# Kernel tuning notes

Measured on AMD Instinct MI355X. Metric: run time of the kernel, lower is better.

## Reference

```python
import jax, jax.numpy as jnp
import numpy as np
from jax import lax

SIGMA1, SIGMA2, TRUNCATE = 4.2, 96.0, 4.0


def _gauss_kernel1d(sigma, truncate):
    # scipy-style: radius = int(truncate*sigma + 0.5), normalized Gaussian
    r = int(truncate * sigma + 0.5)
    t = jnp.arange(-r, r + 1, dtype=jnp.float32)
    k = jnp.exp(-0.5 * (t / sigma) ** 2)
    return k / jnp.sum(k)


def _depthwise_conv1d_centered(x_bcl, k):
    # x_bcl: [B, C, L]; k: [K] with K odd. Centered 'same' conv with reflect padding.
    B, C, L = x_bcl.shape
    K = k.shape[0]
    r = (K - 1) // 2
    xp = jnp.pad(x_bcl, ((0, 0), (0, 0), (r, r)), mode='reflect')
    w = jnp.broadcast_to(k[None, None, :], (C, 1, K)).astype(x_bcl.dtype)
    return lax.conv_general_dilated(
        xp, w, window_strides=(1,), padding='VALID',
        feature_group_count=C,
        dimension_numbers=('NCH', 'OIH', 'NCH'))


def setup_inputs() -> dict:
    key = jax.random.key(0)
    x = jax.random.normal(key, (32, 4096, 321), dtype=jnp.float32)  # [B, L, C]
    return {"x": x}


def reference(x) -> jnp.ndarray:
    k1 = _gauss_kernel1d(SIGMA1, TRUNCATE).astype(x.dtype)
    k2 = _gauss_kernel1d(SIGMA2, TRUNCATE).astype(x.dtype)
    x_bcl = jnp.transpose(x, (0, 2, 1))          # [B, C, L]
    y1 = _depthwise_conv1d_centered(x_bcl, k1)   # narrow Gaussian LP
    y2 = _depthwise_conv1d_centered(x_bcl, k2)   # wide Gaussian LP
    seasonal = y1 - y2
    return jnp.transpose(seasonal, (0, 2, 1))    # back to [B, L, C]
```

## Files before the change

### kernel.cpp

```cpp
#include <hip/hip_runtime.h>
#include <math.h>


#define Bdim 32
#define Ldim 4096
#define Cdim 321

#define R1 17
#define K1n 35
#define R2 384
#define K2n 769

#define GA_R 48
#define GA_N 97
#define GB_R 24
#define GB_N 49

#define NG 257
#define NJD 305
#define NGRP_A 20
#define NSEG 128
#define NTJ 33

#define GA_OFF 0
#define GB_OFF 128
#define W1_OFF 192
#define K2_OFF 256
#define K2P_OFF 1088
#define E2_OFF 4096
#define D_OFF 4096
#define E_OFF (D_OFF + Bdim*NJD*Cdim)
#define WS_TOT (E_OFF + Bdim*NG*Cdim)

__device__ __forceinline__ int mirror_idx(int a) {
    a = a < 0 ? -a : a;
    a = a > (Ldim - 1) ? 2 * (Ldim - 1) - a : a;
    return a;
}

__device__ __forceinline__ int xcd_swizzle(int bid, int nwg) {
    int q = nwg >> 3, r = nwg & 7;
    int xcd = bid & 7, i = bid >> 3;
    int base = (xcd < r) ? xcd * (q + 1) : r * (q + 1) + (xcd - r) * q;
    return base + i;
}

__device__ __forceinline__ float block_sum_1024(float v, float* partial) {
#pragma unroll
    for (int off = 32; off >= 1; off >>= 1) v += __shfl_down(v, off, 64);
    __syncthreads();
    if ((threadIdx.x & 63) == 0) partial[threadIdx.x >> 6] = v;
    __syncthreads();
    float s = partial[0];
#pragma unroll
    for (int i = 1; i < 16; ++i) s += partial[i];
    return s;
}

__global__ void init_weights_kernel(float* __restrict__ w) {
    __shared__ float partial[16];
    const int tid = threadIdx.x;

    {
        float v = 0.f;
        if (tid < GA_N) { float t = (float)(tid - GA_R) * (1.0f / 12.0f); v = expf(-0.5f * t * t); }
        float s = block_sum_1024(v, partial);
        if (tid < GA_N) w[GA_OFF + tid] = v / s;
    }
    {
        const float sb = sqrtf(96.f * 96.f - 12.f * 12.f) * (1.0f / 16.0f);
        float v = 0.f;
        if (tid < GB_N) { float t = (float)(tid - GB_R) / sb; v = expf(-0.5f * t * t); }
        float s = block_sum_1024(v, partial);
        if (tid < GB_N) w[GB_OFF + tid] = v / s;
    }
    {
        float v = 0.f;
        if (tid < K1n) { float t = (float)(tid - R1) * (1.0f / 4.2f); v = expf(-0.5f * t * t); }
        float s = block_sum_1024(v, partial);
        if (tid < K1n) w[W1_OFF + tid] = v / s;
    }
    {
        float v = 0.f;
        if (tid < K2n) { float t = (float)(tid - R2) * (1.0f / 96.0f); v = expf(-0.5f * t * t); }
        float s = block_sum_1024(v, partial);
        if (tid < K2n) w[K2_OFF + tid] = v / s;
        if (tid < 784) w[K2P_OFF + tid] = (tid < K2n) ? v / s : 0.f;
    }
}

__global__ __launch_bounds__(256) void decimA_kernel(
        const float* __restrict__ x, const float* __restrict__ ga,
        float* __restrict__ d) {
    __shared__ float gs[GA_N];
    if (threadIdx.x < GA_N) gs[threadIdx.x] = ga[threadIdx.x];
    __syncthreads();

    const int lb = xcd_swizzle(blockIdx.x, gridDim.x);
    const int lin = lb * 256 + threadIdx.x;
    const int c = lin % Cdim;
    const int rest = lin / Cdim;
    const int g = rest % NGRP_A;
    const int b = rest / NGRP_A;
    if (b >= Bdim) return;

    const int jj0 = -24 + 16 * g;
    const float* xb = x + b * (Ldim * Cdim) + c;

    float acc[16];
#pragma unroll
    for (int ii = 0; ii < 16; ++ii) acc[ii] = 0.f;

    const bool interior = (jj0 >= 3) && (jj0 <= 237);

#pragma unroll 1
    for (int p = 0; p < 16; ++p) {
        float row[22];
        if (interior) {
            const float* xp = xb + (16 * (jj0 - 3) + p) * Cdim;
#pragma unroll
            for (int i = 0; i < 22; ++i) row[i] = xp[i * (16 * Cdim)];
        } else {
#pragma unroll
            for (int i = 0; i < 22; ++i)
                row[i] = xb[mirror_idx(16 * (jj0 - 3 + i) + p) * Cdim];
        }
#pragma unroll
        for (int q = 0; q < 6; ++q) {
            const float wq = gs[16 * q + p];
#pragma unroll
            for (int ii = 0; ii < 16; ++ii)
                acc[ii] = fmaf(wq, row[ii + q], acc[ii]);
        }
        if (p == 0) {
            const float w6 = gs[96];
#pragma unroll
            for (int ii = 0; ii < 16; ++ii)
                acc[ii] = fmaf(w6, row[ii + 6], acc[ii]);
        }
    }

    const int j0d = jj0 + 24;
    float* db = d + (b * NJD + j0d) * Cdim + c;
#pragma unroll
    for (int ii = 0; ii < 16; ++ii)
        if (j0d + ii < NJD) db[ii * Cdim] = acc[ii];
}

__global__ __launch_bounds__(256) void coarseB_kernel(
        const float* __restrict__ d, const float* __restrict__ gb,
        float* __restrict__ e) {
    __shared__ float gbs[GB_N];
    if (threadIdx.x < GB_N) gbs[threadIdx.x] = gb[threadIdx.x];
    __syncthreads();

    const int lin = blockIdx.x * 256 + threadIdx.x;
    const int c = lin % Cdim;
    const int rest = lin / Cdim;
    const int tj = rest % NTJ;
    const int b = rest / NTJ;
    if (b >= Bdim) return;

    const int j0 = tj * 8;
    const float* db = d + b * (NJD * Cdim) + c;

    float row[56];
#pragma unroll
    for (int r = 0; r < 56; ++r) {
        int idx = j0 + r;
        idx = idx > (NJD - 1) ? (NJD - 1) : idx;
        row[r] = db[idx * Cdim];
    }

    float acc[8];
#pragma unroll
    for (int jj = 0; jj < 8; ++jj) acc[jj] = 0.f;
#pragma unroll
    for (int s = 0; s < GB_N; ++s) {
        const float wv = gbs[s];
#pragma unroll
        for (int jj = 0; jj < 8; ++jj)
            acc[jj] = fmaf(wv, row[s + jj], acc[jj]);
    }

    float* eb = e + (b * NG + j0) * Cdim + c;
#pragma unroll
    for (int jj = 0; jj < 8; ++jj)
        if (j0 + jj < NG) eb[jj * Cdim] = acc[jj];
}

__global__ __launch_bounds__(256, 2) void narrow_kernel(
        const float* __restrict__ x, const float* __restrict__ w1,
        const float* __restrict__ e, float* __restrict__ out) {
    __shared__ float ws[K1n];
    if (threadIdx.x < K1n) ws[threadIdx.x] = w1[threadIdx.x];
    __syncthreads();

    const int lb = xcd_swizzle(blockIdx.x, gridDim.x);
    const int lin = lb * 256 + threadIdx.x;
    const int c = lin % Cdim;
    const int rest = lin / Cdim;
    const int seg = rest % NSEG;
    const int b = rest / NSEG;
    if (b >= Bdim) return;

    const int l0 = seg * 32;
    const float* xb = x + b * (Ldim * Cdim) + c;

    const int j0 = seg * 2;
    const float* eb = e + (b * NG + j0) * Cdim + c;
    const float z0 = eb[0];
    const float z1 = eb[Cdim];
    const float z2 = eb[2 * Cdim];

    float row[66];
    if (seg >= 1 && seg <= 126) {
        const float* xp = xb + (l0 - R1) * Cdim;
#pragma unroll
        for (int i = 0; i < 66; ++i) row[i] = xp[i * Cdim];
    } else {
#pragma unroll
        for (int i = 0; i < 66; ++i)
            row[i] = xb[mirror_idx(l0 - R1 + i) * Cdim];
    }

    float acc[32];
#pragma unroll
    for (int m = 0; m < 32; ++m) acc[m] = 0.f;
#pragma unroll
    for (int t = 0; t < K1n; ++t) {
        const float wt = ws[t];
#pragma unroll
        for (int m = 0; m < 32; ++m)
            acc[m] = fmaf(wt, row[t + m], acc[m]);
    }

    const float d0 = (z1 - z0) * (1.0f / 16.0f);
    const float d1 = (z2 - z1) * (1.0f / 16.0f);
    float* ob = out + (b * Ldim + l0) * Cdim + c;
#pragma unroll
    for (int m = 0; m < 16; ++m)
        ob[m * Cdim] = acc[m] - fmaf(d0, (float)m, z0);
#pragma unroll
    for (int m = 16; m < 32; ++m)
        ob[m * Cdim] = acc[m] - fmaf(d1, (float)(m - 16), z1);
}

#define JPT 16
#define NJG 17
__global__ __launch_bounds__(256, 2) void wide_mid_kernel(
        const float* __restrict__ x, const float* __restrict__ w2p,
        float* __restrict__ z) {
    __shared__ float w2s[784];
    for (int i = threadIdx.x; i < 784; i += 256) w2s[i] = w2p[i];
    __syncthreads();

    const int gid = blockIdx.x * 256 + threadIdx.x;
    const int c = gid % Cdim;
    const int rest = gid / Cdim;
    const int jg = rest % NJG;
    const int b = rest / NJG;
    if (b >= Bdim) return;

    const int j0 = jg * JPT;
    const float* xb = x + b * (Ldim * Cdim) + c;

    float acc[JPT];
#pragma unroll
    for (int jj = 0; jj < JPT; ++jj) acc[jj] = 0.f;

    const bool interior = (j0 >= 24) && (16 * (j0 + 39) + 15 <= Ldim - 1);

#pragma unroll 1
    for (int p = 0; p < 16; ++p) {
        float row[64];
        if (interior) {
            const float* xp = xb + (16 * (j0 - 24) + p) * Cdim;
#pragma unroll
            for (int i = 0; i < 64; ++i) row[i] = xp[i * (16 * Cdim)];
        } else {
#pragma unroll
            for (int i = 0; i < 64; ++i)
                row[i] = xb[mirror_idx(16 * (j0 - 24 + i) + p) * Cdim];
        }
#pragma unroll
        for (int q = 0; q < 49; ++q) {
            const float wq = w2s[q * 16 + p];
#pragma unroll
            for (int jj = 0; jj < JPT; ++jj)
                acc[jj] = fmaf(wq, row[q + jj], acc[jj]);
        }
    }

    float* zb = z + (b * NG + j0) * Cdim + c;
#pragma unroll
    for (int jj = 0; jj < JPT; ++jj)
        if (j0 + jj < NG) zb[jj * Cdim] = acc[jj];
}

__global__ __launch_bounds__(256) void naive_kernel(
        const float* __restrict__ x, const float* __restrict__ w,
        float* __restrict__ out) {
    const int gid = blockIdx.x * 256 + threadIdx.x;
    if (gid >= Bdim * Ldim * Cdim) return;
    const int c = gid % Cdim;
    const int rest = gid / Cdim;
    const int l = rest % Ldim;
    const int b = rest / Ldim;
    const float* xb = x + b * (Ldim * Cdim) + c;
    float a2 = 0.f, a1 = 0.f;
    for (int t = 0; t < K2n; ++t)
        a2 = fmaf(w[K2_OFF + t], xb[mirror_idx(l + t - R2) * Cdim], a2);
#pragma unroll
    for (int t = 0; t < K1n; ++t)
        a1 = fmaf(w[W1_OFF + t], xb[mirror_idx(l + t - R1) * Cdim], a1);
    out[gid] = a1 - a2;
}

extern "C" void kernel_launch(void* const* d_in, const int* in_sizes, int n_in,
                              void* d_out, int out_size, void* d_ws, size_t ws_size,
                              hipStream_t stream) {
    (void)in_sizes; (void)n_in; (void)out_size;
    const float* x = (const float*)d_in[0];
    float* out = (float*)d_out;
    float* w = (float*)d_ws;

    hipLaunchKernelGGL(init_weights_kernel, dim3(1), dim3(1024), 0, stream, w);

    const size_t need_pyr = (size_t)WS_TOT * sizeof(float);
    const size_t need_mid = (size_t)(E2_OFF + Bdim * NG * Cdim) * sizeof(float);

    const int nar_total = Bdim * NSEG * Cdim;
    const dim3 nar_grid((nar_total + 255) / 256);

    if (ws_size >= need_pyr) {
        const int a_total = Bdim * NGRP_A * Cdim;
        hipLaunchKernelGGL(decimA_kernel, dim3((a_total + 255) / 256), dim3(256),
                           0, stream, x, w + GA_OFF, w + D_OFF);
        const int b_total = Bdim * NTJ * Cdim;
        hipLaunchKernelGGL(coarseB_kernel, dim3((b_total + 255) / 256), dim3(256),
                           0, stream, w + D_OFF, w + GB_OFF, w + E_OFF);
        hipLaunchKernelGGL(narrow_kernel, nar_grid, dim3(256),
                           0, stream, x, w + W1_OFF, w + E_OFF, out);
    } else if (ws_size >= need_mid) {
        const int wide_total = Bdim * NJG * Cdim;
        hipLaunchKernelGGL(wide_mid_kernel, dim3((wide_total + 255) / 256), dim3(256),
                           0, stream, x, w + K2P_OFF, w + E2_OFF);
        hipLaunchKernelGGL(narrow_kernel, nar_grid, dim3(256),
                           0, stream, x, w + W1_OFF, w + E2_OFF, out);
    } else {
        const int total = Bdim * Ldim * Cdim;
        hipLaunchKernelGGL(naive_kernel, dim3((total + 255) / 256), dim3(256),
                           0, stream, x, w, out);
    }
}
```

Before: 150.4 us.

## Stage narrow-filter input tiles in LDS via direct global-to-LDS loads

Replaces the narrow-filter kernel on the pyramid path with a tiled version. Each block stages a 66-row by 128-channel window of x into shared memory, using global_load_lds for the aligned channel tiles and a plain loop for the 65-channel tail. Each thread then computes 8 outputs for two channels with packed float2 FMAs from a register window. The wide-band value is linearly interpolated from the coarse pyramid level. This removes the redundant per-output global reads of the 35-tap window, at the cost of LDS use and higher register pressure.

```diff
diff --git a/kernel.cpp b/kernel.cpp
--- a/kernel.cpp
+++ b/kernel.cpp
@@ -19,8 +19,14 @@
 #define NG 257
 #define NJD 305
 #define NGRP_A 20
+#define NTJ 33
+
+#define TLN 32
+#define WR 66
+#define LSTR 128
+#define NLG3 128
+#define NCT3 3
 #define NSEG 128
-#define NTJ 33
 
 #define GA_OFF 0
 #define GB_OFF 128
@@ -32,6 +38,8 @@
 #define E_OFF (D_OFF + Bdim*NJD*Cdim)
 #define WS_TOT (E_OFF + Bdim*NG*Cdim)
 
+typedef float f32x2 __attribute__((ext_vector_type(2)));
+
 __device__ __forceinline__ int mirror_idx(int a) {
     a = a < 0 ? -a : a;
     a = a > (Ldim - 1) ? 2 * (Ldim - 1) - a : a;
@@ -189,7 +197,114 @@
         if (j0 + jj < NG) eb[jj * Cdim] = acc[jj];
 }
 
-__global__ __launch_bounds__(256, 2) void narrow_kernel(
+__global__ __launch_bounds__(256) void narrow_v10_kernel(
+        const float* __restrict__ x, const float* __restrict__ w1,
+        const float* __restrict__ e, float* __restrict__ out) {
+    __shared__ float ws[K1n];
+    __shared__ float tile[WR * LSTR];
+    if (threadIdx.x < K1n) ws[threadIdx.x] = w1[threadIdx.x];
+
+    const int bid = xcd_swizzle(blockIdx.x, gridDim.x);
+    const int ct = bid % NCT3;
+    const int rest = bid / NCT3;
+    const int lg = rest % NLG3;
+    const int b = rest / NLG3;
+
+    const int c0 = ct * 128;
+    const int l0 = lg * TLN;
+    const int lbase = l0 - R1;
+    const int lane = threadIdx.x & 63;
+    const int wv = threadIdx.x >> 6;
+    const float* xb = x + (size_t)b * (Ldim * Cdim);
+
+    if (ct < 2) {
+        const int rsel = (lane >> 5);
+        const int coff = (lane & 31) * 4;
+#pragma unroll
+        for (int k = 0; k < 9; ++k) {
+            const int p = wv + 4 * k;
+            if (p < 33) {
+                const int grow = mirror_idx(lbase + 2 * p + rsel);
+                const float* g = xb + (size_t)grow * Cdim + c0 + coff;
+                __builtin_amdgcn_global_load_lds(
+                    (const __attribute__((address_space(1))) void*)g,
+                    (__attribute__((address_space(3))) void*)(&tile[2 * p * LSTR]),
+                    16, 0, 0);
+            }
+        }
+    } else {
+#pragma unroll 1
+        for (int i = threadIdx.x; i < WR * 65; i += 256) {
+            const int r = i / 65;
+            const int cc = i - r * 65;
+            tile[r * LSTR + cc] = xb[(size_t)mirror_idx(lbase + r) * Cdim + 256 + cc];
+        }
+    }
+    __syncthreads();
+
+    const int cp = threadIdx.x & 63;
+    const int lgrp = threadIdx.x >> 6;
+    const int lg8 = lgrp * 8;
+    const int j = (l0 >> 4) + (lgrp >> 1);
+    const float f0 = (float)((lgrp & 1) * 8);
+
+    if (ct < 2 || cp < 32) {
+        f32x2 r2[42];
+#pragma unroll
+        for (int i = 0; i < 42; ++i)
+            r2[i] = *reinterpret_cast<const f32x2*>(&tile[(lg8 + i) * LSTR + 2 * cp]);
+
+        f32x2 acc[8];
+#pragma unroll
+        for (int m = 0; m < 8; ++m) acc[m] = (f32x2)(0.f);
+#pragma unroll
+        for (int t = 0; t < K1n; ++t) {
+            const float wt = ws[t];
+            const f32x2 w2 = {wt, wt};
+#pragma unroll
+            for (int m = 0; m < 8; ++m)
+                acc[m] = __builtin_elementwise_fma(w2, r2[t + m], acc[m]);
+        }
+
+        const int ce = c0 + 2 * cp;
+        const float* eb = e + ((size_t)b * NG + j) * Cdim + ce;
+        const float z0x = eb[0],    z0y = eb[1];
+        const float z1x = eb[Cdim], z1y = eb[Cdim + 1];
+        const float dzx = (z1x - z0x) * 0.0625f;
+        const float dzy = (z1y - z0y) * 0.0625f;
+
+        float* ob = out + ((size_t)b * Ldim + l0 + lg8) * Cdim + ce;
+#pragma unroll
+        for (int m = 0; m < 8; ++m) {
+            const float fm = f0 + (float)m;
+            ob[m * Cdim]     = acc[m].x - fmaf(dzx, fm, z0x);
+            ob[m * Cdim + 1] = acc[m].y - fmaf(dzy, fm, z0y);
+        }
+    } else if (cp == 32) {
+        float rs[42];
+#pragma unroll
+        for (int i = 0; i < 42; ++i) rs[i] = tile[(lg8 + i) * LSTR + 64];
+        float acc[8];
+#pragma unroll
+        for (int m = 0; m < 8; ++m) acc[m] = 0.f;
+#pragma unroll
+        for (int t = 0; t < K1n; ++t) {
+            const float wt = ws[t];
+#pragma unroll
+            for (int m = 0; m < 8; ++m)
+                acc[m] = fmaf(wt, rs[t + m], acc[m]);
+        }
+        const float z0 = e[((size_t)b * NG + j) * Cdim + 320];
+        const float z1 = e[((size_t)b * NG + j + 1) * Cdim + 320];
+        const float dz = (z1 - z0) * 0.0625f;
+        float* ob = out + ((size_t)b * Ldim + l0 + lg8) * Cdim + 320;
+#pragma unroll
+        for (int m = 0; m < 8; ++m)
+            ob[m * Cdim] = acc[m] - fmaf(dz, f0 + (float)m, z0);
+    }
+}
+
+__global__ __launch_bounds__(256, 2) void narrow_reg_kernel(
         const float* __restrict__ x, const float* __restrict__ w1,
         const float* __restrict__ e, float* __restrict__ out) {
     __shared__ float ws[K1n];
@@ -330,9 +445,6 @@
     const size_t need_pyr = (size_t)WS_TOT * sizeof(float);
     const size_t need_mid = (size_t)(E2_OFF + Bdim * NG * Cdim) * sizeof(float);
 
-    const int nar_total = Bdim * NSEG * Cdim;
-    const dim3 nar_grid((nar_total + 255) / 256);
-
     if (ws_size >= need_pyr) {
         const int a_total = Bdim * NGRP_A * Cdim;
         hipLaunchKernelGGL(decimA_kernel, dim3((a_total + 255) / 256), dim3(256),
@@ -340,13 +452,15 @@
         const int b_total = Bdim * NTJ * Cdim;
         hipLaunchKernelGGL(coarseB_kernel, dim3((b_total + 255) / 256), dim3(256),
                            0, stream, w + D_OFF, w + GB_OFF, w + E_OFF);
-        hipLaunchKernelGGL(narrow_kernel, nar_grid, dim3(256),
+        const int nblk = Bdim * NLG3 * NCT3;
+        hipLaunchKernelGGL(narrow_v10_kernel, dim3(nblk), dim3(256),
                            0, stream, x, w + W1_OFF, w + E_OFF, out);
     } else if (ws_size >= need_mid) {
         const int wide_total = Bdim * NJG * Cdim;
         hipLaunchKernelGGL(wide_mid_kernel, dim3((wide_total + 255) / 256), dim3(256),
                            0, stream, x, w + K2P_OFF, w + E2_OFF);
-        hipLaunchKernelGGL(narrow_kernel, nar_grid, dim3(256),
+        const int nar_total = Bdim * NSEG * Cdim;
+        hipLaunchKernelGGL(narrow_reg_kernel, dim3((nar_total + 255) / 256), dim3(256),
                            0, stream, x, w + W1_OFF, w + E2_OFF, out);
     } else {
         const int total = Bdim * Ldim * Cdim;
```

New measurement: 161.6 us. 7.4% more time.
